# Kernel tuning notes

Measured on AMD Instinct MI355X. Metric: run time of the kernel, lower is better.

Reference implementation:

```python
import jax, jax.numpy as jnp
import numpy as np

N_U, N_V, E, D = 100000, 100000, 600000, 128


def setup_inputs() -> dict:
    key = jax.random.key(0)
    ks = jax.random.split(key, 8)
    Eu = jax.random.normal(ks[0], (N_U, D), dtype=jnp.float32)
    Ev = jax.random.normal(ks[1], (N_V, D), dtype=jnp.float32)
    # small-scale weights so distances stay in a numerically sane range
    W1 = jax.random.normal(ks[2], (D, D), dtype=jnp.float32) * 0.05
    b1 = jax.random.normal(ks[3], (D,), dtype=jnp.float32) * 0.05
    W2 = jax.random.normal(ks[4], (D, D), dtype=jnp.float32) * 0.05
    b2 = jax.random.normal(ks[5], (D,), dtype=jnp.float32) * 0.05
    edge_index = jax.random.randint(ks[6], (2, E), 0, N_U, dtype=jnp.int64)
    edge_val = jax.random.uniform(ks[7], (E,), dtype=jnp.float32)
    return {"Eu": Eu, "Ev": Ev, "W1": W1, "b1": b1, "W2": W2, "b2": b2,
            "edge_index": edge_index, "edge_val": edge_val}


def reference(Eu, Ev, W1, b1, W2, b2, edge_index, edge_val):
    # fc1 / fc2: Linear + ReLU (torch Linear applies x @ W^T + b)
    tu = jax.nn.relu(Eu @ W1.T + b1)   # [N_U, D]
    tv = jax.nn.relu(Ev @ W2.T + b2)   # [N_V, D]
    src, dst = edge_index[0], edge_index[1]
    diff = tu[src] - tv[dst]                     # [E, D] edge-wise gather
    distances = jnp.sqrt(jnp.sum(diff * diff, axis=1))  # L2 norm per edge
    similarities = jnp.exp(distances)
    Ag = edge_val * jax.nn.sigmoid(similarities)  # values of sparse output
    return Ag
```

## Files before the change

### kernel.cpp

```cpp
#include <hip/hip_runtime.h>
#include <hip/hip_fp16.h>

typedef _Float16 half4 __attribute__((ext_vector_type(4)));
typedef float floatx4 __attribute__((ext_vector_type(4)));

#define LDSW 136

__global__ __launch_bounds__(256) void gemm_relu_kernel(
    const float* __restrict__ Xu, const float* __restrict__ Xv,
    const float* __restrict__ W1, const float* __restrict__ W2,
    const float* __restrict__ b1, const float* __restrict__ b2,
    _Float16* __restrict__ OUTu, _Float16* __restrict__ OUTv,
    int Nu, int Nv)
{
  const float* X; const float* W; const float* bias; _Float16* OUT; int N;
  if (blockIdx.y == 0) { X = Xu; W = W1; bias = b1; OUT = OUTu; N = Nu; }
  else                 { X = Xv; W = W2; bias = b2; OUT = OUTv; N = Nv; }

  __shared__ _Float16 Wl[128 * LDSW];

  const int tid = threadIdx.x;
  for (int c = tid; c < 4096; c += 256) {
    floatx4 v = *(const floatx4*)(W + c * 4);
    half4 h;
    h[0] = (_Float16)v[0]; h[1] = (_Float16)v[1];
    h[2] = (_Float16)v[2]; h[3] = (_Float16)v[3];
    const int t = (c * 4) >> 7;
    const int k = (c * 4) & 127;
    *(half4*)(&Wl[t * LDSW + k]) = h;
  }
  __syncthreads();

  const int wave = tid >> 6;
  const int lane = tid & 63;
  const int r16  = lane & 15;
  const int g4   = lane >> 4;
  const long rowBase = (long)blockIdx.x * 256 + wave * 64;

  float bv[8];
  #pragma unroll
  for (int t = 0; t < 8; ++t) bv[t] = bias[t * 16 + r16];

  for (int grp = 0; grp < 4; ++grp) {
    const long rowA = rowBase + grp * 16 + r16;
    const float* xr = X + (rowA < N ? rowA : 0) * 128;

    floatx4 acc[8];
    #pragma unroll
    for (int t = 0; t < 8; ++t) acc[t] = (floatx4){0.f, 0.f, 0.f, 0.f};

    #pragma unroll
    for (int kk = 0; kk < 8; ++kk) {
      const int kbase = kk * 16 + g4 * 4;
      floatx4 xa = *(const floatx4*)(xr + kbase);
      half4 a;
      a[0] = (_Float16)xa[0]; a[1] = (_Float16)xa[1];
      a[2] = (_Float16)xa[2]; a[3] = (_Float16)xa[3];
      #pragma unroll
      for (int t = 0; t < 8; ++t) {
        half4 b = *(const half4*)(&Wl[(t * 16 + r16) * LDSW + kbase]);
        acc[t] = __builtin_amdgcn_mfma_f32_16x16x16f16(a, b, acc[t], 0, 0, 0);
      }
    }

    const long rr0 = rowBase + grp * 16 + g4 * 4;
    #pragma unroll
    for (int j = 0; j < 4; ++j) {
      const long rr = rr0 + j;
      if (rr < N) {
        #pragma unroll
        for (int t = 0; t < 8; ++t) {
          float v = acc[t][j] + bv[t];
          v = v > 0.f ? v : 0.f;
          OUT[rr * 128 + t * 16 + r16] = (_Float16)v;
        }
      }
    }
  }
}

__global__ __launch_bounds__(256) void edge_kernel(
    const _Float16* __restrict__ tu, const _Float16* __restrict__ tv,
    const int* __restrict__ eidx, const float* __restrict__ eval_,
    float* __restrict__ out, int E)
{
  const long t = (long)blockIdx.x * 256 + threadIdx.x;
  const long e = t >> 4;
  const int sub = (int)(t & 15);
  if (e >= E) return;

  const int src = eidx[e];
  const int dst = eidx[E + e];

  floatx4 va = *(const floatx4*)(tu + (long)src * 128 + sub * 8);
  floatx4 vb = *(const floatx4*)(tv + (long)dst * 128 + sub * 8);

  const __half2* ha = (const __half2*)&va;
  const __half2* hb = (const __half2*)&vb;
  float s = 0.f;
  #pragma unroll
  for (int j = 0; j < 4; ++j) {
    float2 fa = __half22float2(ha[j]);
    float2 fb = __half22float2(hb[j]);
    float d0 = fa.x - fb.x;
    float d1 = fa.y - fb.y;
    s += d0 * d0 + d1 * d1;
  }
  #pragma unroll
  for (int off = 1; off < 16; off <<= 1)
    s += __shfl_xor(s, off, 64);

  if (sub == 0) {
    float dist = sqrtf(s);
    float sim  = expf(dist);
    float sig  = 1.f / (1.f + expf(-sim));
    out[e] = eval_[e] * sig;
  }
}

extern "C" void kernel_launch(void* const* d_in, const int* in_sizes, int n_in,
                              void* d_out, int out_size, void* d_ws, size_t ws_size,
                              hipStream_t stream) {
  const float* Eu  = (const float*)d_in[0];
  const float* Ev  = (const float*)d_in[1];
  const float* W1  = (const float*)d_in[2];
  const float* b1  = (const float*)d_in[3];
  const float* W2  = (const float*)d_in[4];
  const float* b2  = (const float*)d_in[5];
  const int*  eidx = (const int*)d_in[6];
  const float* ev  = (const float*)d_in[7];
  float* out = (float*)d_out;

  const int Nu = in_sizes[0] / 128;
  const int Nv = in_sizes[1] / 128;
  const int E  = in_sizes[7];

  _Float16* tu = (_Float16*)d_ws;
  _Float16* tv = tu + (size_t)Nu * 128;

  const int nmax = Nu > Nv ? Nu : Nv;
  dim3 ggrid((nmax + 255) / 256, 2);
  gemm_relu_kernel<<<ggrid, 256, 0, stream>>>(Eu, Ev, W1, W2, b1, b2, tu, tv, Nu, Nv);

  const long ethreads = (long)E * 16;
  const int eblocks = (int)((ethreads + 255) / 256);
  edge_kernel<<<eblocks, 256, 0, stream>>>(tu, tv, eidx, ev, out, E);
}
```

Before: 218.2 us.

## Compute transposed GEMM tile to vectorize output stores and drop LDS weight staging

The GEMM kernel now computes the transposed product, with W rows as the A operand and X rows as the B operand. Each lane then holds four consecutive output features of one row and can write a packed half4 store instead of scattered 2-byte stores. Weights are read straight from global memory (L2/L1-cached) instead of being staged into LDS, which removes the shared-memory fill and the barrier. Each block now covers 64 rows instead of 256, giving 4x more blocks, with a launch-bounds occupancy hint. The cost is redundant global reads of W in every wave, where the old code amortized one LDS fill over 256 rows.

```diff
diff --git a/kernel.cpp b/kernel.cpp
--- a/kernel.cpp
+++ b/kernel.cpp
@@ -4,9 +4,7 @@
 typedef _Float16 half4 __attribute__((ext_vector_type(4)));
 typedef float floatx4 __attribute__((ext_vector_type(4)));
 
-#define LDSW 136
-
-__global__ __launch_bounds__(256) void gemm_relu_kernel(
+__global__ __launch_bounds__(256, 5) void gemm_relu_kernel(
     const float* __restrict__ Xu, const float* __restrict__ Xv,
     const float* __restrict__ W1, const float* __restrict__ W2,
     const float* __restrict__ b1, const float* __restrict__ b2,
@@ -17,64 +15,54 @@
   if (blockIdx.y == 0) { X = Xu; W = W1; bias = b1; OUT = OUTu; N = Nu; }
   else                 { X = Xv; W = W2; bias = b2; OUT = OUTv; N = Nv; }
 
-  __shared__ _Float16 Wl[128 * LDSW];
-
-  const int tid = threadIdx.x;
-  for (int c = tid; c < 4096; c += 256) {
-    floatx4 v = *(const floatx4*)(W + c * 4);
-    half4 h;
-    h[0] = (_Float16)v[0]; h[1] = (_Float16)v[1];
-    h[2] = (_Float16)v[2]; h[3] = (_Float16)v[3];
-    const int t = (c * 4) >> 7;
-    const int k = (c * 4) & 127;
-    *(half4*)(&Wl[t * LDSW + k]) = h;
-  }
-  __syncthreads();
-
+  const int tid  = threadIdx.x;
   const int wave = tid >> 6;
   const int lane = tid & 63;
   const int r16  = lane & 15;
   const int g4   = lane >> 4;
-  const long rowBase = (long)blockIdx.x * 256 + wave * 64;
 
-  float bv[8];
+  const long n = (long)blockIdx.x * 64 + wave * 16 + r16;
+  const float* xr = X + (n < N ? n : 0) * 128;
+
+  half4 bf[8];
   #pragma unroll
-  for (int t = 0; t < 8; ++t) bv[t] = bias[t * 16 + r16];
+  for (int kk = 0; kk < 8; ++kk) {
+    floatx4 v = *(const floatx4*)(xr + kk * 16 + g4 * 4);
+    half4 h;
+    h[0] = (_Float16)v[0]; h[1] = (_Float16)v[1];
+    h[2] = (_Float16)v[2]; h[3] = (_Float16)v[3];
+    bf[kk] = h;
+  }
 
-  for (int grp = 0; grp < 4; ++grp) {
-    const long rowA = rowBase + grp * 16 + r16;
-    const float* xr = X + (rowA < N ? rowA : 0) * 128;
+  floatx4 acc[8];
+  #pragma unroll
+  for (int t = 0; t < 8; ++t) acc[t] = (floatx4){0.f, 0.f, 0.f, 0.f};
 
-    floatx4 acc[8];
-    #pragma unroll
-    for (int t = 0; t < 8; ++t) acc[t] = (floatx4){0.f, 0.f, 0.f, 0.f};
-
+  #pragma unroll
+  for (int tt = 0; tt < 8; ++tt) {
+    const float* wr = W + (size_t)(tt * 16 + r16) * 128;
     #pragma unroll
     for (int kk = 0; kk < 8; ++kk) {
-      const int kbase = kk * 16 + g4 * 4;
-      floatx4 xa = *(const floatx4*)(xr + kbase);
+      floatx4 v = *(const floatx4*)(wr + kk * 16 + g4 * 4);
       half4 a;
-      a[0] = (_Float16)xa[0]; a[1] = (_Float16)xa[1];
-      a[2] = (_Float16)xa[2]; a[3] = (_Float16)xa[3];
+      a[0] = (_Float16)v[0]; a[1] = (_Float16)v[1];
+      a[2] = (_Float16)v[2]; a[3] = (_Float16)v[3];
+      acc[tt] = __builtin_amdgcn_mfma_f32_16x16x16f16(a, bf[kk], acc[tt], 0, 0, 0);
+    }
+  }
+
+  if (n < N) {
+    _Float16* orow = OUT + n * 128;
+    #pragma unroll
+    for (int tt = 0; tt < 8; ++tt) {
+      floatx4 bv = *(const floatx4*)(bias + tt * 16 + g4 * 4);
+      half4 h;
       #pragma unroll
-      for (int t = 0; t < 8; ++t) {
-        half4 b = *(const half4*)(&Wl[(t * 16 + r16) * LDSW + kbase]);
-        acc[t] = __builtin_amdgcn_mfma_f32_16x16x16f16(a, b, acc[t], 0, 0, 0);
+      for (int j = 0; j < 4; ++j) {
+        float x = acc[tt][j] + bv[j];
+        h[j] = (_Float16)(x > 0.f ? x : 0.f);
       }
-    }
-
-    const long rr0 = rowBase + grp * 16 + g4 * 4;
-    #pragma unroll
-    for (int j = 0; j < 4; ++j) {
-      const long rr = rr0 + j;
-      if (rr < N) {
-        #pragma unroll
-        for (int t = 0; t < 8; ++t) {
-          float v = acc[t][j] + bv[t];
-          v = v > 0.f ? v : 0.f;
-          OUT[rr * 128 + t * 16 + r16] = (_Float16)v;
-        }
-      }
+      *(half4*)(orow + tt * 16 + g4 * 4) = h;
     }
   }
 }
@@ -139,7 +127,7 @@
   _Float16* tv = tu + (size_t)Nu * 128;
 
   const int nmax = Nu > Nv ? Nu : Nv;
-  dim3 ggrid((nmax + 255) / 256, 2);
+  dim3 ggrid((nmax + 63) / 64, 2);
   gemm_relu_kernel<<<ggrid, 256, 0, stream>>>(Eu, Ev, W1, W2, b1, b2, tu, tv, Nu, Nv);
 
   const long ethreads = (long)E * 16;
```

Measured after the change: 270.9 us. 24.2% more time.
